# Optimization experiments

Hardware: AMD Instinct MI355X
Metric: run time of the kernel (lower is better)

The kernel has to match this reference:

```python
import jax, jax.numpy as jnp
import numpy as np

B, H, W = 8, 1024, 1280
EPS = 1e-7
MIN_DEPTH, MAX_DEPTH = 10.0, 255.0


def _constants(batch, view_to_syn='left'):
    trans = np.array([-4.14339018, -0.0238197036, -0.00190685259], np.float32)
    K_u = np.array([1035.30811, 0.0, 596.955017, 0.0, 1035.08765, 520.410034, 0.0, 0.0, 1.0], np.float32).reshape(3, 3)
    K_u[0, :] /= 1280.0
    K_u[1, :] /= 1024.0
    K_u4 = np.zeros((4, 4), np.float32); K_u4[:3, :3] = K_u; K_u4[3, 3] = 1.0
    K_d = np.array([1035.17419, 0.0, 688.361877, 0.0, 1034.979, 521.070801, 0.0, 0.0, 1.0], np.float32).reshape(3, 3)
    K_d[0, :] /= 1280.0
    K_d[1, :] /= 1024.0
    K_d4 = np.zeros((4, 4), np.float32); K_d4[:3, :3] = K_d; K_d4[3, 3] = 1.0
    if view_to_syn == 'right':
        src, tgt, t = K_u4, K_d4, trans
    else:
        src, tgt, t = K_d4, K_u4, -trans
    source_K = jnp.asarray(np.tile(src[None], (batch, 1, 1)))
    target_K = jnp.asarray(np.tile(tgt[None], (batch, 1, 1)))
    trans_vec = jnp.asarray(np.tile(t[None], (batch, 1)))
    return source_K, target_K, trans_vec


def setup_inputs() -> dict:
    key = jax.random.key(0)
    k1, k2 = jax.random.split(key)
    img = jax.random.normal(k1, (B, 3, H, W), jnp.float32)
    pred_disp = jax.random.uniform(k2, (B, 1, H, W), jnp.float32)
    source_K, target_K, trans_vec = _constants(B, 'left')
    return {"img": img, "pred_disp": pred_disp, "source_K": source_K,
            "target_K": target_K, "trans_vec": trans_vec}


def _grid_sample_border(img, grid):
    """Bilinear grid_sample, padding_mode='border', align_corners=False (torch default).
    img: [B,C,H,W], grid: [B,H,W,2] in [-1,1] (x,y). Returns [B,C,H,W]."""
    b, c, h, w = img.shape
    x = (grid[..., 0] + 1.0) * w * 0.5 - 0.5  # [B,H,W]
    y = (grid[..., 1] + 1.0) * h * 0.5 - 0.5
    x0f = jnp.floor(x); y0f = jnp.floor(y)
    wx = (x - x0f)[:, None]  # [B,1,H,W]
    wy = (y - y0f)[:, None]
    x0 = jnp.clip(x0f.astype(jnp.int32), 0, w - 1)
    x1 = jnp.clip(x0f.astype(jnp.int32) + 1, 0, w - 1)
    y0 = jnp.clip(y0f.astype(jnp.int32), 0, h - 1)
    y1 = jnp.clip(y0f.astype(jnp.int32) + 1, 0, h - 1)
    gather = jax.vmap(lambda im, yi, xi: im[:, yi, xi])  # -> [B,C,H,W]
    i00 = gather(img, y0, x0)
    i01 = gather(img, y0, x1)
    i10 = gather(img, y1, x0)
    i11 = gather(img, y1, x1)
    return (i00 * (1 - wx) * (1 - wy) + i01 * wx * (1 - wy)
            + i10 * (1 - wx) * wy + i11 * wx * wy)


def reference(img, pred_disp, source_K, target_K, trans_vec):
    b, _, h, w = img.shape
    # disp -> depth
    min_disp, max_disp = 1.0 / MAX_DEPTH, 1.0 / MIN_DEPTH
    scaled_disp = min_disp + (max_disp - min_disp) * pred_disp
    depth = 1.0 / scaled_disp  # [B,1,H,W]
    # homogeneous pixel grid [3, H*W]
    xs, ys = jnp.meshgrid(jnp.arange(w, dtype=jnp.float32),
                          jnp.arange(h, dtype=jnp.float32), indexing='xy')
    pix = jnp.stack([xs.reshape(-1), ys.reshape(-1), jnp.ones(h * w, jnp.float32)], 0)
    # backproject
    inv_K = jnp.linalg.inv(source_K)[:, :3, :3]  # [B,3,3]
    cam = jnp.einsum('bij,jn->bin', inv_K, pix) * depth.reshape(b, 1, -1)  # [B,3,HW]
    cam4 = jnp.concatenate([cam, jnp.ones((b, 1, h * w), cam.dtype)], axis=1)  # [B,4,HW]
    # extrinsic: R = I, so T @ R = translation matrix
    T = jnp.tile(jnp.eye(4, dtype=img.dtype)[None], (b, 1, 1)).at[:, :3, 3].set(trans_vec.reshape(b, 3))
    P = jnp.matmul(target_K, T)[:, :3, :]  # [B,3,4]
    cp = jnp.matmul(P, cam4)  # [B,3,HW]
    pc = cp[:, :2] / (cp[:, 2:3] + EPS)  # [B,2,HW]
    pc = pc.reshape(b, 2, h, w).transpose(0, 2, 3, 1)  # [B,H,W,2]
    scale = jnp.array([w - 1, h - 1], dtype=pc.dtype)
    grid = (pc / scale - 0.5) * 2.0
    return _grid_sample_border(img, grid)
```

## Files before the change

kernel.cpp:

```cpp
#include <hip/hip_runtime.h>

#define BB 8
#define HH 1024
#define WW 1280
#define HW (HH * WW)
#define EPSF 1e-7f

#define TH 16
#define TCOLS 264
#define SROWS 18
#define CPR 66
#define CHUNKS (3 * SROWS * CPR)
#define CH_PAD 3584

typedef float f4 __attribute__((ext_vector_type(4)));

__device__ __forceinline__ float fast_rcp(float x) {
    float r = __builtin_amdgcn_rcpf(x);
    r = r * __builtin_fmaf(-x, r, 2.0f);
    return r;
}

__global__ void precompute_consts(
    const float* __restrict__ srcK, const float* __restrict__ tgtK,
    const float* __restrict__ trans, float* __restrict__ cb)
{
    const int b = threadIdx.x;
    if (b >= BB) return;
    const float* sK = srcK + b * 16;
    const float* tK = tgtK + b * 16;
    const float* tv = trans + b * 3;

    const float fsx = sK[0], csx = sK[2];
    const float fsy = sK[5], csy = sK[6];
    const float ftx = tK[0], ctx = tK[2];
    const float fty = tK[5], cty = tK[6];
    const float t0 = tv[0], t1 = tv[1], t2 = tv[2];

    const float Sx = (float)WW / (float)(WW - 1);
    const float Sy = (float)HH / (float)(HH - 1);
    const float rfsx = 1.0f / fsx;
    const float rfsy = 1.0f / fsy;
    float* c = cb + b * 8;
    c[0] = ftx * rfsx * Sx;
    c[1] = __builtin_fmaf(-ftx * csx, rfsx, ctx) * Sx;
    c[2] = (ftx * t0 + ctx * t2) * Sx;
    c[3] = fty * rfsy * Sy;
    c[4] = __builtin_fmaf(-fty * csy, rfsy, cty) * Sy;
    c[5] = (fty * t1 + cty * t2) * Sy;
    c[6] = t2 + EPSF;
    c[7] = 0.0f;
}

__global__ __launch_bounds__(256) void synth_view_kernel(
    const float* __restrict__ img, const float* __restrict__ disp,
    const float* __restrict__ cbuf, float* __restrict__ out)
{
    __shared__ __align__(16) float st[CH_PAD * 4];

    const int tid = threadIdx.x;
    const int wid = blockIdx.x;
    const int r   = wid & 7;
    int q = wid >> 3;
    const int tyl = q & 7;  q >>= 3;
    const int xb  = q % 5;
    const int b   = q / 5;
    const int y0  = (r * 8 + tyl) * TH;
    const int x0  = xb * 256;
    const int x   = x0 + tid;

    const float* imb = img + (size_t)b * 3 * HW;

    float dsp[TH];
#pragma unroll
    for (int j = 0; j < TH; ++j)
        dsp[j] = __builtin_nontemporal_load(
            disp + (size_t)b * HW + (size_t)(y0 + j) * WW + x);

    f4 v[14];
#pragma unroll
    for (int i = 0; i < 14; ++i) {
        const int qq = i * 256 + tid;
        const int qc = min(qq, CHUNKS - 1);
        const int c  = qc / (SROWS * CPR);
        const int rm = qc - c * (SROWS * CPR);
        const int ri = rm / CPR;
        const int k  = rm - ri * CPR;
        const int row = min(max(y0 - 1 + ri, 0), HH - 1);
        const int col = min(max(x0 - 4 + 4 * k, 0), WW - 4);
        v[i] = *reinterpret_cast<const f4*>(imb + (size_t)(c * HH + row) * WW + col);
    }
#pragma unroll
    for (int i = 0; i < 14; ++i) {
        const int qq = i * 256 + tid;
        *reinterpret_cast<f4*>(&st[qq * 4]) = v[i];
    }

    const float* cb = cbuf + b * 8;
    const float A00 = cb[0], A02 = cb[1], C0 = cb[2];
    const float A11 = cb[3], A12 = cb[4], C1 = cb[5];
    const float t2e = cb[6];

    const float mind = 1.0f / 255.0f;
    const float rng  = 0.1f - mind;
    const float axc  = __builtin_fmaf(A00, (float)x, A02);

    __syncthreads();

    float* outb = out + (size_t)b * 3 * HW + x;

#pragma unroll
    for (int j = 0; j < TH; ++j) {
        const int y = y0 + j;
        const float sd  = __builtin_fmaf(dsp[j], rng, mind);
        const float rrz = fast_rcp(__builtin_fmaf(t2e, sd, 1.0f));
        const float ayc = __builtin_fmaf(A11, (float)y, A12);
        const float sx  = __builtin_fmaf(__builtin_fmaf(C0, sd, axc), rrz, -0.5f);
        const float sy  = __builtin_fmaf(__builtin_fmaf(C1, sd, ayc), rrz, -0.5f);

        const int ixc = min(max((int)floorf(sx), 0), WW - 2);
        const int iyc = min(max((int)floorf(sy), 0), HH - 2);
        const float wx = fminf(fmaxf(sx - (float)ixc, 0.0f), 1.0f);
        const float wy = fminf(fmaxf(sy - (float)iyc, 0.0f), 1.0f);

        const int wcol = min(max(ixc - x0 + 4, 0), TCOLS - 2);
        const int wrow = min(max(iyc - y0 + 1, 0), SROWS - 2);

        const float wxm = 1.0f - wx, wym = 1.0f - wy;
        const float w00 = wxm * wym, w01 = wx * wym;
        const float w10 = wxm * wy,  w11 = wx * wy;

        const int base = wrow * TCOLS + wcol;
#pragma unroll
        for (int c = 0; c < 3; ++c) {
            const float* p = &st[(c * SROWS) * TCOLS + base];
            float acc =          p[0]         * w00;
            acc = __builtin_fmaf(p[1],         w01, acc);
            acc = __builtin_fmaf(p[TCOLS],     w10, acc);
            acc = __builtin_fmaf(p[TCOLS + 1], w11, acc);
            __builtin_nontemporal_store(acc, outb + (size_t)c * HW + (size_t)y * WW);
        }
    }
}

extern "C" void kernel_launch(void* const* d_in, const int* in_sizes, int n_in,
                              void* d_out, int out_size, void* d_ws, size_t ws_size,
                              hipStream_t stream) {
    const float* img   = (const float*)d_in[0];
    const float* disp  = (const float*)d_in[1];
    const float* srcK  = (const float*)d_in[2];
    const float* tgtK  = (const float*)d_in[3];
    const float* trans = (const float*)d_in[4];
    float* out = (float*)d_out;
    float* cb  = (float*)d_ws;

    precompute_consts<<<dim3(1), dim3(64), 0, stream>>>(srcK, tgtK, trans, cb);

    dim3 block(256, 1, 1);
    dim3 grid(5 * 64 * BB, 1, 1);
    synth_view_kernel<<<grid, block, 0, stream>>>(img, disp, cb, out);
}
```

Baseline: 249.4 us.

## Stage image tile per channel via direct global-to-LDS loads for higher occupancy

Instead of loading all three channels of the image tile through registers into a large LDS buffer, the kernel now stages one channel at a time. It uses the `global_load_lds` builtin, which copies global memory straight into LDS, with a smaller buffer, and adds a launch-bounds occupancy hint. Sampling offsets and bilinear weights are computed once per pixel row and reused across the three channel passes. The aim is to cut register and LDS pressure so more blocks fit per CU. The cost is extra barriers that serialise the per-channel load and compute phases.

```diff
diff --git a/kernel.cpp b/kernel.cpp
--- a/kernel.cpp
+++ b/kernel.cpp
@@ -10,10 +10,12 @@
 #define TCOLS 264
 #define SROWS 18
 #define CPR 66
-#define CHUNKS (3 * SROWS * CPR)
-#define CH_PAD 3584
+#define CCH (SROWS * CPR)
+#define CPT 5
+#define STF (CPT * 256 * 4)
 
-typedef float f4 __attribute__((ext_vector_type(4)));
+#define GAS __attribute__((address_space(1)))
+#define LAS __attribute__((address_space(3)))
 
 __device__ __forceinline__ float fast_rcp(float x) {
     float r = __builtin_amdgcn_rcpf(x);
@@ -52,11 +54,11 @@
     c[7] = 0.0f;
 }
 
-__global__ __launch_bounds__(256) void synth_view_kernel(
+__global__ __launch_bounds__(256, 7) void synth_view_kernel(
     const float* __restrict__ img, const float* __restrict__ disp,
     const float* __restrict__ cbuf, float* __restrict__ out)
 {
-    __shared__ __align__(16) float st[CH_PAD * 4];
+    __shared__ __align__(16) float st[STF];
 
     const int tid = threadIdx.x;
     const int wid = blockIdx.x;
@@ -71,30 +73,29 @@
 
     const float* imb = img + (size_t)b * 3 * HW;
 
+    int goff[CPT];
+#pragma unroll
+    for (int i = 0; i < CPT; ++i) {
+        const int qq = i * 256 + tid;
+        const int qc = min(qq, CCH - 1);
+        const int ri = qc / CPR;
+        const int k  = qc - ri * CPR;
+        const int row = min(max(y0 - 1 + ri, 0), HH - 1);
+        const int col = min(max(x0 - 4 + 4 * k, 0), WW - 4);
+        goff[i] = row * WW + col;
+    }
+
+#pragma unroll
+    for (int i = 0; i < CPT; ++i)
+        __builtin_amdgcn_global_load_lds(
+            (const GAS unsigned int*)(const void*)(imb + goff[i]),
+            (LAS unsigned int*)(void*)&st[(i * 256 + tid) * 4], 16, 0, 0);
+
+    const float* db = disp + (size_t)b * HW + (size_t)y0 * WW + x;
     float dsp[TH];
 #pragma unroll
     for (int j = 0; j < TH; ++j)
-        dsp[j] = __builtin_nontemporal_load(
-            disp + (size_t)b * HW + (size_t)(y0 + j) * WW + x);
-
-    f4 v[14];
-#pragma unroll
-    for (int i = 0; i < 14; ++i) {
-        const int qq = i * 256 + tid;
-        const int qc = min(qq, CHUNKS - 1);
-        const int c  = qc / (SROWS * CPR);
-        const int rm = qc - c * (SROWS * CPR);
-        const int ri = rm / CPR;
-        const int k  = rm - ri * CPR;
-        const int row = min(max(y0 - 1 + ri, 0), HH - 1);
-        const int col = min(max(x0 - 4 + 4 * k, 0), WW - 4);
-        v[i] = *reinterpret_cast<const f4*>(imb + (size_t)(c * HH + row) * WW + col);
-    }
-#pragma unroll
-    for (int i = 0; i < 14; ++i) {
-        const int qq = i * 256 + tid;
-        *reinterpret_cast<f4*>(&st[qq * 4]) = v[i];
-    }
+        dsp[j] = __builtin_nontemporal_load(db + j * WW);
 
     const float* cb = cbuf + b * 8;
     const float A00 = cb[0], A02 = cb[1], C0 = cb[2];
@@ -105,10 +106,7 @@
     const float rng  = 0.1f - mind;
     const float axc  = __builtin_fmaf(A00, (float)x, A02);
 
-    __syncthreads();
-
-    float* outb = out + (size_t)b * 3 * HW + x;
-
+    int   lb[TH]; float wxa[TH], wya[TH];
 #pragma unroll
     for (int j = 0; j < TH; ++j) {
         const int y = y0 + j;
@@ -120,25 +118,37 @@
 
         const int ixc = min(max((int)floorf(sx), 0), WW - 2);
         const int iyc = min(max((int)floorf(sy), 0), HH - 2);
-        const float wx = fminf(fmaxf(sx - (float)ixc, 0.0f), 1.0f);
-        const float wy = fminf(fmaxf(sy - (float)iyc, 0.0f), 1.0f);
-
+        wxa[j] = fminf(fmaxf(sx - (float)ixc, 0.0f), 1.0f);
+        wya[j] = fminf(fmaxf(sy - (float)iyc, 0.0f), 1.0f);
         const int wcol = min(max(ixc - x0 + 4, 0), TCOLS - 2);
         const int wrow = min(max(iyc - y0 + 1, 0), SROWS - 2);
+        lb[j] = (wrow * TCOLS + wcol) * 4;
+    }
 
-        const float wxm = 1.0f - wx, wym = 1.0f - wy;
-        const float w00 = wxm * wym, w01 = wx * wym;
-        const float w10 = wxm * wy,  w11 = wx * wy;
+    float* outb = out + (size_t)b * 3 * HW + (size_t)y0 * WW + x;
 
-        const int base = wrow * TCOLS + wcol;
+    for (int c = 0; c < 3; ++c) {
+        if (c > 0) {
+            __syncthreads();
 #pragma unroll
-        for (int c = 0; c < 3; ++c) {
-            const float* p = &st[(c * SROWS) * TCOLS + base];
-            float acc =          p[0]         * w00;
-            acc = __builtin_fmaf(p[1],         w01, acc);
-            acc = __builtin_fmaf(p[TCOLS],     w10, acc);
-            acc = __builtin_fmaf(p[TCOLS + 1], w11, acc);
-            __builtin_nontemporal_store(acc, outb + (size_t)c * HW + (size_t)y * WW);
+            for (int i = 0; i < CPT; ++i)
+                __builtin_amdgcn_global_load_lds(
+                    (const GAS unsigned int*)(const void*)(imb + (size_t)c * HW + goff[i]),
+                    (LAS unsigned int*)(void*)&st[(i * 256 + tid) * 4], 16, 0, 0);
+        }
+        __syncthreads();
+
+        float* oc = outb + (size_t)c * HW;
+#pragma unroll
+        for (int j = 0; j < TH; ++j) {
+            const float* p = (const float*)((const char*)st + lb[j]);
+            const float wx = wxa[j], wy = wya[j];
+            const float wxm = 1.0f - wx, wym = 1.0f - wy;
+            float acc =          p[0]         * (wxm * wym);
+            acc = __builtin_fmaf(p[1],         wx * wym, acc);
+            acc = __builtin_fmaf(p[TCOLS],     wxm * wy, acc);
+            acc = __builtin_fmaf(p[TCOLS + 1], wx * wy,  acc);
+            __builtin_nontemporal_store(acc, oc + j * WW);
         }
     }
 }
```

Measured after the change: 310.2 us. +24.4%, slower.

## Shrink tiles to one row per block and stage halo via direct-to-LDS loads

Applied to the files above, without the earlier changes.

Each block now produces a single output row instead of a 16-row tile. It stages only the three input rows y-1..y+1 per channel into LDS, using global_load_lds asynchronous copies instead of register-staged vector loads. The grid grows sixteenfold, and per-row disparity and projection math is computed once per thread. This cuts LDS footprint and register pressure to allow more resident blocks, but each input row is now fetched about three times instead of roughly 1.1 times. The sampling window is also narrowed to ±1 row, which relies on the vertical displacement staying within one pixel.

```diff
diff --git a/kernel.cpp b/kernel.cpp
--- a/kernel.cpp
+++ b/kernel.cpp
@@ -6,14 +6,13 @@
 #define HW (HH * WW)
 #define EPSF 1e-7f
 
-#define TH 16
 #define TCOLS 264
-#define SROWS 18
-#define CPR 66
-#define CHUNKS (3 * SROWS * CPR)
-#define CH_PAD 3584
+#define CPR   66
+#define CCH   (3 * 3 * CPR)
+#define CHROW (3 * TCOLS)
 
-typedef float f4 __attribute__((ext_vector_type(4)));
+#define GAS __attribute__((address_space(1)))
+#define LAS __attribute__((address_space(3)))
 
 __device__ __forceinline__ float fast_rcp(float x) {
     float r = __builtin_amdgcn_rcpf(x);
@@ -56,45 +55,42 @@
     const float* __restrict__ img, const float* __restrict__ disp,
     const float* __restrict__ cbuf, float* __restrict__ out)
 {
-    __shared__ __align__(16) float st[CH_PAD * 4];
+    __shared__ __align__(16) float st[768 * 4];
 
     const int tid = threadIdx.x;
     const int wid = blockIdx.x;
     const int r   = wid & 7;
     int q = wid >> 3;
-    const int tyl = q & 7;  q >>= 3;
+    const int yl  = q & 127;  q >>= 7;
     const int xb  = q % 5;
     const int b   = q / 5;
-    const int y0  = (r * 8 + tyl) * TH;
+    const int y   = r * 128 + yl;
     const int x0  = xb * 256;
     const int x   = x0 + tid;
 
     const float* imb = img + (size_t)b * 3 * HW;
 
-    float dsp[TH];
+    const float dsp = __builtin_nontemporal_load(
+        disp + (size_t)b * HW + (size_t)y * WW + x);
+
+    const int ym = min(max(y - 1, 0), HH - 1);
+    const int y0c = max(y - 1, 0);
+    const int y2c = min(y + 1, HH - 1);
 #pragma unroll
-    for (int j = 0; j < TH; ++j)
-        dsp[j] = __builtin_nontemporal_load(
-            disp + (size_t)b * HW + (size_t)(y0 + j) * WW + x);
-
-    f4 v[14];
-#pragma unroll
-    for (int i = 0; i < 14; ++i) {
+    for (int i = 0; i < 3; ++i) {
         const int qq = i * 256 + tid;
-        const int qc = min(qq, CHUNKS - 1);
-        const int c  = qc / (SROWS * CPR);
-        const int rm = qc - c * (SROWS * CPR);
-        const int ri = rm / CPR;
-        const int k  = rm - ri * CPR;
-        const int row = min(max(y0 - 1 + ri, 0), HH - 1);
+        const int qc = min(qq, CCH - 1);
+        const int ch = (qc >= 396) ? 2 : ((qc >= 198) ? 1 : 0);
+        const int rm = qc - ch * 198;
+        const int rw = (rm >= 132) ? 2 : ((rm >= 66) ? 1 : 0);
+        const int k  = rm - rw * 66;
+        const int row = (rw == 0) ? y0c : ((rw == 1) ? y : y2c);
         const int col = min(max(x0 - 4 + 4 * k, 0), WW - 4);
-        v[i] = *reinterpret_cast<const f4*>(imb + (size_t)(c * HH + row) * WW + col);
+        __builtin_amdgcn_global_load_lds(
+            (const GAS unsigned int*)(const void*)(imb + (size_t)(ch * HH + row) * WW + col),
+            (LAS unsigned int*)(void*)&st[qq * 4], 16, 0, 0);
     }
-#pragma unroll
-    for (int i = 0; i < 14; ++i) {
-        const int qq = i * 256 + tid;
-        *reinterpret_cast<f4*>(&st[qq * 4]) = v[i];
-    }
+    (void)ym;
 
     const float* cb = cbuf + b * 8;
     const float A00 = cb[0], A02 = cb[1], C0 = cb[2];
@@ -103,43 +99,37 @@
 
     const float mind = 1.0f / 255.0f;
     const float rng  = 0.1f - mind;
+    const float sd   = __builtin_fmaf(dsp, rng, mind);
+    const float rrz  = fast_rcp(__builtin_fmaf(t2e, sd, 1.0f));
     const float axc  = __builtin_fmaf(A00, (float)x, A02);
+    const float ayc  = __builtin_fmaf(A11, (float)y, A12);
+    const float sx   = __builtin_fmaf(__builtin_fmaf(C0, sd, axc), rrz, -0.5f);
+    const float sy   = __builtin_fmaf(__builtin_fmaf(C1, sd, ayc), rrz, -0.5f);
+
+    const int ixc = min(max((int)floorf(sx), 0), WW - 2);
+    const int iyc = min(max((int)floorf(sy), 0), HH - 2);
+    const float wx = fminf(fmaxf(sx - (float)ixc, 0.0f), 1.0f);
+    const float wy = fminf(fmaxf(sy - (float)iyc, 0.0f), 1.0f);
+
+    const int wcol = min(max(ixc - x0 + 4, 0), TCOLS - 2);
+    const int wrow = min(max(iyc - y + 1, 0), 1);
+    const int base = wrow * TCOLS + wcol;
+
+    const float wxm = 1.0f - wx, wym = 1.0f - wy;
+    const float w00 = wxm * wym, w01 = wx * wym;
+    const float w10 = wxm * wy,  w11 = wx * wy;
 
     __syncthreads();
 
-    float* outb = out + (size_t)b * 3 * HW + x;
-
+    float* outb = out + (size_t)b * 3 * HW + (size_t)y * WW + x;
 #pragma unroll
-    for (int j = 0; j < TH; ++j) {
-        const int y = y0 + j;
-        const float sd  = __builtin_fmaf(dsp[j], rng, mind);
-        const float rrz = fast_rcp(__builtin_fmaf(t2e, sd, 1.0f));
-        const float ayc = __builtin_fmaf(A11, (float)y, A12);
-        const float sx  = __builtin_fmaf(__builtin_fmaf(C0, sd, axc), rrz, -0.5f);
-        const float sy  = __builtin_fmaf(__builtin_fmaf(C1, sd, ayc), rrz, -0.5f);
-
-        const int ixc = min(max((int)floorf(sx), 0), WW - 2);
-        const int iyc = min(max((int)floorf(sy), 0), HH - 2);
-        const float wx = fminf(fmaxf(sx - (float)ixc, 0.0f), 1.0f);
-        const float wy = fminf(fmaxf(sy - (float)iyc, 0.0f), 1.0f);
-
-        const int wcol = min(max(ixc - x0 + 4, 0), TCOLS - 2);
-        const int wrow = min(max(iyc - y0 + 1, 0), SROWS - 2);
-
-        const float wxm = 1.0f - wx, wym = 1.0f - wy;
-        const float w00 = wxm * wym, w01 = wx * wym;
-        const float w10 = wxm * wy,  w11 = wx * wy;
-
-        const int base = wrow * TCOLS + wcol;
-#pragma unroll
-        for (int c = 0; c < 3; ++c) {
-            const float* p = &st[(c * SROWS) * TCOLS + base];
-            float acc =          p[0]         * w00;
-            acc = __builtin_fmaf(p[1],         w01, acc);
-            acc = __builtin_fmaf(p[TCOLS],     w10, acc);
-            acc = __builtin_fmaf(p[TCOLS + 1], w11, acc);
-            __builtin_nontemporal_store(acc, outb + (size_t)c * HW + (size_t)y * WW);
-        }
+    for (int c = 0; c < 3; ++c) {
+        const float* p = &st[c * CHROW + base];
+        float acc =          p[0]          * w00;
+        acc = __builtin_fmaf(p[1],          w01, acc);
+        acc = __builtin_fmaf(p[TCOLS],      w10, acc);
+        acc = __builtin_fmaf(p[TCOLS + 1],  w11, acc);
+        __builtin_nontemporal_store(acc, outb + (size_t)c * HW);
     }
 }
 
@@ -157,6 +147,6 @@
     precompute_consts<<<dim3(1), dim3(64), 0, stream>>>(srcK, tgtK, trans, cb);
 
     dim3 block(256, 1, 1);
-    dim3 grid(5 * 64 * BB, 1, 1);
+    dim3 grid(5 * 1024 * BB, 1, 1);
     synth_view_kernel<<<grid, block, 0, stream>>>(img, disp, cb, out);
 }
```

New measurement: 253.7 us. Within noise of the previous version (+1.7%).
